# Optimization experiments

Measured on AMD Instinct MI355X. Metric: run time of the kernel, lower is better.

The kernel has to match this reference:

```python
import jax, jax.numpy as jnp
import numpy as np

N_NODES = 50000
N_EDGES = 800000
N_ENT = 500000
N_REL = 500
L = 2          # num_layers
H = 8          # head_num
D = 16         # per-head dim (hidden_dim // head_num)
HID = H * D    # 128
IN = 128       # in_ent_dim == in_rel_dim == hidden_dim
B = 64         # number of graphs in the batch
SLOPE = 0.2    # leaky-relu negative slope


def setup_inputs() -> dict:
    key = jax.random.key(0)
    ks = jax.random.split(key, 11)
    return {
        "ent_table": jax.random.normal(ks[0], (N_ENT, IN), jnp.float32) * 0.05,
        "rel_table": jax.random.normal(ks[1], (N_REL, IN), jnp.float32) * 0.05,
        "W_ent": jax.random.normal(ks[2], (L, IN, HID), jnp.float32) * 0.05,
        "W_rel": jax.random.normal(ks[3], (L, IN, HID), jnp.float32) * 0.05,
        "attn_l": jax.random.normal(ks[4], (L, H, D), jnp.float32) * 0.05,
        "attn_r": jax.random.normal(ks[5], (L, H, D), jnp.float32) * 0.05,
        "attn_e": jax.random.normal(ks[6], (L, H, D), jnp.float32) * 0.05,
        "ent_ids": jax.random.randint(ks[7], (N_NODES,), 0, N_ENT, jnp.int32),
        "rel_ids": jax.random.randint(ks[8], (N_EDGES,), 0, N_REL, jnp.int32),
        "src": jax.random.randint(ks[9], (N_EDGES,), 0, N_NODES, jnp.int32),
        "dst": jax.random.randint(ks[10], (N_EDGES,), 0, N_NODES, jnp.int32),
        # node-0 offset of each subgraph in the batched graph
        "graph_offsets": jnp.arange(B, dtype=jnp.int32) * (N_NODES // B),
    }


def _kge_layer(h, rel_f, src, dst, W_e, W_r, a_l, a_r, a_e):
    # GAT-style relation-aware message passing (KGELayer)
    feat = (h @ W_e).reshape(-1, H, D)        # [N,H,D]
    rfeat = (rel_f @ W_r).reshape(-1, H, D)   # [E,H,D]
    el = jnp.einsum('nhd,hd->nh', feat, a_l)  # src score
    er = jnp.einsum('nhd,hd->nh', feat, a_r)  # dst score
    ee = jnp.einsum('ehd,hd->eh', rfeat, a_e) # relation score
    e = jax.nn.leaky_relu(el[src] + er[dst] + ee, SLOPE)  # [E,H]
    # segment softmax over incoming edges of each dst node
    emax = jax.ops.segment_max(e, dst, num_segments=N_NODES)
    ex = jnp.exp(e - emax[dst])
    denom = jax.ops.segment_sum(ex, dst, num_segments=N_NODES)
    alpha = ex / denom[dst]                   # [E,H]
    msg = (feat[src] + rfeat) * alpha[:, :, None]  # [E,H,D]
    out = jax.ops.segment_sum(msg, dst, num_segments=N_NODES)  # [N,H,D]
    return out.reshape(-1, HID)


def reference(ent_table, rel_table, W_ent, W_rel, attn_l, attn_r, attn_e,
              ent_ids, rel_ids, src, dst, graph_offsets):
    h = ent_table[ent_ids]       # [N,IN]
    rel_f = rel_table[rel_ids]   # [E,IN]
    for l in range(L):
        h = _kge_layer(h, rel_f, src, dst, W_ent[l], W_rel[l],
                       attn_l[l], attn_r[l], attn_e[l])
    # CLS embedding: node 0 of each unbatched subgraph
    return h[graph_offsets]      # [B,HID]
```

## Files before the change

kernel.cpp:

```cpp
#include <hip/hip_runtime.h>
#include <hip/hip_bf16.h>


#define NN   50000
#define NE   800000
#define NR   500
#define HH   8
#define DD   16
#define HIDD 128
#define BB   64

#define MAXS1 16448
#define MAXS0 50000
#define MAXD1 256
#define MAXD2 256


__global__ void k_init(int* slot2, int* slot1, int* slot0, int* c1, int* c2,
                       int* counters) {
    int i = blockIdx.x * blockDim.x + threadIdx.x;
    int stride = gridDim.x * blockDim.x;
    for (int n = i; n < NN; n += stride) { slot2[n] = -1; slot1[n] = -1; slot0[n] = -1; }
    for (int n = i; n < MAXS1; n += stride) c1[n] = 0;
    if (i < BB) c2[i] = 0;
    if (i < 8) counters[i] = 0;
}

__global__ void k_seed(const int* goffs, int* slot2, int* slot1, int* nodesS1,
                       int* counters) {
    int i = threadIdx.x;
    if (i < BB) {
        int n = goffs[i];
        slot2[n] = i;
        slot1[n] = -2;
        nodesS1[i] = n;
    }
    if (i == 0) counters[0] = BB;
}

#define NBUF 512
__global__ void k_scan(const int* __restrict__ src, const int* __restrict__ dst,
                       const int* __restrict__ slotHit, int* __restrict__ slotNew,
                       int* __restrict__ ebuck, int maxd, int* __restrict__ cursor,
                       int* nodes, int nodesCap, int* counters, int cntN) {
    __shared__ int lN[NBUF];
    __shared__ int cNsh, baseN;
    if (threadIdx.x == 0) cNsh = 0;
    __syncthreads();
    int per = (NE + gridDim.x - 1) / gridDim.x;
    int lo = blockIdx.x * per;
    int hi = lo + per; if (hi > NE) hi = NE;
    for (int base = lo; base < hi; base += blockDim.x) {
        int e = base + threadIdx.x;
        if (e < hi) {
            int d = dst[e];
            int slot = slotHit[d];
            if (slot >= 0) {
                int pos = atomicAdd(&cursor[slot], 1);
                if (pos < maxd) ebuck[slot * maxd + pos] = e;
                int s = src[e];
                int old = atomicCAS(&slotNew[s], -1, -2);
                if (old == -1) {
                    int p2 = atomicAdd(&cNsh, 1);
                    lN[p2] = s;
                }
            }
        }
        __syncthreads();
        if (cNsh >= NBUF - 256) {
            int nN = cNsh;
            if (threadIdx.x == 0) baseN = atomicAdd(&counters[cntN], nN);
            __syncthreads();
            for (int i = threadIdx.x; i < nN; i += blockDim.x) {
                int g = baseN + i; if (g < nodesCap) nodes[g] = lN[i];
            }
            __syncthreads();
            if (threadIdx.x == 0) cNsh = 0;
        }
        __syncthreads();
    }
    int nN = cNsh;
    if (threadIdx.x == 0) baseN = atomicAdd(&counters[cntN], nN);
    __syncthreads();
    for (int i = threadIdx.x; i < nN; i += blockDim.x) {
        int g = baseN + i; if (g < nodesCap) nodes[g] = lN[i];
    }
}

__global__ void k_finS1(int* slot1, const int* nodesS1, int* slot0, int* nodesS0,
                        int* counters) {
    int k = blockIdx.x * blockDim.x + threadIdx.x;
    int cnt = counters[0]; if (cnt > MAXS1) cnt = MAXS1;
    if (k < cnt) {
        int n = nodesS1[k];
        slot1[n] = k;
        slot0[n] = -2;
        nodesS0[k] = n;
    }
    if (k == 0) counters[1] = cnt;
}

#define RELB 1000
#define FT 8
__global__ void k_relfeat0(const float* rel_table, const float* __restrict__ W_rel,
                           const float* attn_e, float* rproj, float* ee,
                           const int* nodesS0, const int* counters, const int* ent_ids,
                           const float* __restrict__ ent_table, const float* __restrict__ W_ent,
                           const float* __restrict__ attn_l, const float* __restrict__ attn_r,
                           float* feat0, float* el0, float* er0, int* slot0) {
    int t = threadIdx.x;
    __shared__ float sh[FT][HIDD];
    if (blockIdx.x < RELB) {
        int b = blockIdx.x;
        int l = b / NR, r = b % NR;
        sh[0][t] = rel_table[r * HIDD + t];
        __syncthreads();
        const float* W = W_rel + l * HIDD * HIDD;
        float acc = 0.f;
        for (int j = 0; j < HIDD; j++) acc += sh[0][j] * W[j * HIDD + t];
        rproj[(l * NR + r) * HIDD + t] = acc;
        sh[1][t] = acc;
        __syncthreads();
        if (t < HH) {
            float s = 0.f;
            #pragma unroll
            for (int d = 0; d < DD; d++) s += sh[1][t * DD + d] * attn_e[(l * HH + t) * DD + d];
            ee[(l * NR + r) * HH + t] = s;
        }
        return;
    }
    int cnt = counters[1]; if (cnt > MAXS0) cnt = MAXS0;
    int nTiles = (cnt + FT - 1) / FT;
    int gstride = gridDim.x - RELB;
    for (int tile = blockIdx.x - RELB; tile < nTiles; tile += gstride) {
        int k0 = tile * FT;
        #pragma unroll
        for (int m = 0; m < FT; m++) {
            int k = k0 + m;
            int n = nodesS0[k < cnt ? k : 0];
            if (k < cnt && t == 0) slot0[n] = k;
            sh[m][t] = ent_table[(long)ent_ids[n] * HIDD + t];
        }
        __syncthreads();
        float acc[FT];
        #pragma unroll
        for (int m = 0; m < FT; m++) acc[m] = 0.f;
        for (int j = 0; j < HIDD; j++) {
            float w = W_ent[j * HIDD + t];
            #pragma unroll
            for (int m = 0; m < FT; m++) acc[m] += sh[m][j] * w;
        }
        __syncthreads();
        #pragma unroll
        for (int m = 0; m < FT; m++) {
            int k = k0 + m;
            if (k < cnt) feat0[k * HIDD + t] = acc[m];
            sh[m][t] = acc[m];
        }
        __syncthreads();
        {
            int m = t >> 4, idx = t & 15, h = idx >> 1, isR = idx & 1;
            int k = k0 + m;
            if (k < cnt) {
                const float* av = (isR ? attn_r : attn_l) + h * DD;
                float s = 0.f;
                #pragma unroll
                for (int d = 0; d < DD; d++) s += sh[m][h * DD + d] * av[d];
                if (isR) er0[k * HH + h] = s; else el0[k * HH + h] = s;
            }
        }
        __syncthreads();
    }
}

__global__ void k_layer1(const int* counters,
                         const int* __restrict__ c1, const int* __restrict__ ebuck1,
                         const int* __restrict__ src, const int* __restrict__ rel_ids,
                         const int* __restrict__ slot0,
                         const float* __restrict__ feat0, const float* __restrict__ rproj0,
                         const float* __restrict__ el0, const float* __restrict__ er0,
                         const float* __restrict__ ee0,
                         const float* __restrict__ W_ent1,
                         const float* attn_l1, const float* attn_r1,
                         float* feat1, float* el1, float* er1) {
    int t = threadIdx.x;
    int h = t >> 4;
    int cnt = counters[0]; if (cnt > MAXS1) cnt = MAXS1;
    __shared__ int   eks[MAXD1];
    __shared__ int   erid[MAXD1];
    __shared__ float exsh[MAXD1 * HH];
    __shared__ float row[HIDD];
    __shared__ float f[HIDD];
    for (int k = blockIdx.x; k < cnt; k += gridDim.x) {
        int deg = c1[k]; if (deg > MAXD1) deg = MAXD1;
        for (int i = t; i < deg; i += blockDim.x) {
            int e = ebuck1[k * MAXD1 + i];
            eks[i]  = slot0[src[e]];
            erid[i] = rel_ids[e];
        }
        __syncthreads();
        for (int idx = t; idx < deg * HH; idx += blockDim.x) {
            int i = idx >> 3, hh = idx & 7;
            float sc = el0[eks[i] * HH + hh] + er0[k * HH + hh] + ee0[erid[i] * HH + hh];
            sc = sc >= 0.f ? sc : 0.2f * sc;
            exsh[idx] = expf(sc);
        }
        __syncthreads();
        float acc = 0.f, den = 0.f;
        #pragma unroll 4
        for (int i = 0; i < deg; i++) {
            float ex = exsh[i * HH + h];
            acc += (feat0[eks[i] * HIDD + t] + rproj0[erid[i] * HIDD + t]) * ex;
            den += ex;
        }
        row[t] = den > 0.f ? acc / den : 0.f;
        __syncthreads();
        float a2 = 0.f;
        for (int j = 0; j < HIDD; j++) a2 += row[j] * W_ent1[j * HIDD + t];
        feat1[k * HIDD + t] = a2;
        f[t] = a2;
        __syncthreads();
        if (t < HH) {
            float s = 0.f;
            #pragma unroll
            for (int d = 0; d < DD; d++) s += f[t * DD + d] * attn_l1[t * DD + d];
            el1[k * HH + t] = s;
        } else if (t < 2 * HH) {
            int hh = t - HH;
            float s = 0.f;
            #pragma unroll
            for (int d = 0; d < DD; d++) s += f[hh * DD + d] * attn_r1[hh * DD + d];
            er1[k * HH + hh] = s;
        }
        __syncthreads();
    }
}

__global__ void k_layer2(const int* __restrict__ c2, const int* __restrict__ ebuck2,
                         const int* __restrict__ src, const int* __restrict__ rel_ids,
                         const int* __restrict__ slot1,
                         const float* __restrict__ feat1, const float* __restrict__ rproj1,
                         const float* __restrict__ el1, const float* __restrict__ er1,
                         const float* __restrict__ ee1,
                         float* out) {
    int g = blockIdx.x;
    int t = threadIdx.x;
    int h = t >> 4;
    __shared__ int   eks[MAXD2];
    __shared__ int   erid[MAXD2];
    __shared__ float exsh[MAXD2 * HH];
    int deg = c2[g]; if (deg > MAXD2) deg = MAXD2;
    for (int i = t; i < deg; i += blockDim.x) {
        int e = ebuck2[g * MAXD2 + i];
        eks[i]  = slot1[src[e]];
        erid[i] = rel_ids[e];
    }
    __syncthreads();
    for (int idx = t; idx < deg * HH; idx += blockDim.x) {
        int i = idx >> 3, hh = idx & 7;
        float sc = el1[eks[i] * HH + hh] + er1[g * HH + hh] + ee1[erid[i] * HH + hh];
        sc = sc >= 0.f ? sc : 0.2f * sc;
        exsh[idx] = expf(sc);
    }
    __syncthreads();
    float acc = 0.f, den = 0.f;
    #pragma unroll 4
    for (int i = 0; i < deg; i++) {
        float ex = exsh[i * HH + h];
        acc += (feat1[eks[i] * HIDD + t] + rproj1[erid[i] * HIDD + t]) * ex;
        den += ex;
    }
    out[g * HIDD + t] = den > 0.f ? acc / den : 0.f;
}

extern "C" void kernel_launch(void* const* d_in, const int* in_sizes, int n_in,
                              void* d_out, int out_size, void* d_ws, size_t ws_size,
                              hipStream_t stream) {
    const float* ent_table = (const float*)d_in[0];
    const float* rel_table = (const float*)d_in[1];
    const float* W_ent     = (const float*)d_in[2];
    const float* W_rel     = (const float*)d_in[3];
    const float* attn_l    = (const float*)d_in[4];
    const float* attn_r    = (const float*)d_in[5];
    const float* attn_e    = (const float*)d_in[6];
    const int*   ent_ids   = (const int*)d_in[7];
    const int*   rel_ids   = (const int*)d_in[8];
    const int*   src       = (const int*)d_in[9];
    const int*   dst       = (const int*)d_in[10];
    const int*   goffs     = (const int*)d_in[11];
    float*       out       = (float*)d_out;

    char* p = (char*)d_ws;
    auto alloc = [&](size_t nbytes) {
        void* q = (void*)p;
        p += (nbytes + 255) & ~(size_t)255;
        return q;
    };
    float* rproj   = (float*)alloc((size_t)2 * NR * HIDD * 4);
    float* ee      = (float*)alloc((size_t)2 * NR * HH * 4);
    int*   slot2   = (int*)alloc((size_t)NN * 4);
    int*   slot1   = (int*)alloc((size_t)NN * 4);
    int*   slot0   = (int*)alloc((size_t)NN * 4);
    int*   nodesS1 = (int*)alloc((size_t)MAXS1 * 4);
    int*   nodesS0 = (int*)alloc((size_t)MAXS0 * 4);
    int*   counters= (int*)alloc(8 * 4);
    int*   c1      = (int*)alloc((size_t)MAXS1 * 4);
    int*   c2      = (int*)alloc((size_t)BB * 4);
    int*   ebuck1  = (int*)alloc((size_t)MAXS1 * MAXD1 * 4);
    int*   ebuck2  = (int*)alloc((size_t)BB * MAXD2 * 4);
    float* feat0   = (float*)alloc((size_t)MAXS0 * HIDD * 4);
    float* el0     = (float*)alloc((size_t)MAXS0 * HH * 4);
    float* er0     = (float*)alloc((size_t)MAXS0 * HH * 4);
    float* feat1   = (float*)alloc((size_t)MAXS1 * HIDD * 4);
    float* el1     = (float*)alloc((size_t)MAXS1 * HH * 4);
    float* er1     = (float*)alloc((size_t)MAXS1 * HH * 4);

    const float* rproj0 = rproj;
    const float* rproj1 = rproj + (size_t)NR * HIDD;
    const float* ee0 = ee;
    const float* ee1 = ee + (size_t)NR * HH;
    const float* W_ent0 = W_ent;
    const float* W_ent1 = W_ent + HIDD * HIDD;
    const float* attn_l0 = attn_l, *attn_l1 = attn_l + HH * DD;
    const float* attn_r0 = attn_r, *attn_r1 = attn_r + HH * DD;

    hipLaunchKernelGGL(k_init, dim3(256), dim3(256), 0, stream,
                       slot2, slot1, slot0, c1, c2, counters);
    hipLaunchKernelGGL(k_seed, dim3(1), dim3(64), 0, stream,
                       goffs, slot2, slot1, nodesS1, counters);
    hipLaunchKernelGGL(k_scan, dim3(512), dim3(256), 0, stream,
                       src, dst, slot2, slot1, ebuck2, MAXD2, c2,
                       nodesS1, MAXS1, counters, 0);
    hipLaunchKernelGGL(k_finS1, dim3((MAXS1 + 255) / 256), dim3(256), 0, stream,
                       slot1, nodesS1, slot0, nodesS0, counters);
    hipLaunchKernelGGL(k_scan, dim3(512), dim3(256), 0, stream,
                       src, dst, slot1, slot0, ebuck1, MAXD1, c1,
                       nodesS0, MAXS0, counters, 1);
    hipLaunchKernelGGL(k_relfeat0, dim3(RELB + 1048), dim3(HIDD), 0, stream,
                       rel_table, W_rel, attn_e, rproj, ee,
                       nodesS0, counters, ent_ids, ent_table, W_ent0,
                       attn_l0, attn_r0, feat0, el0, er0, slot0);
    hipLaunchKernelGGL(k_layer1, dim3(1024), dim3(HIDD), 0, stream,
                       counters, c1, ebuck1, src, rel_ids, slot0,
                       feat0, rproj0, el0, er0, ee0, W_ent1, attn_l1, attn_r1,
                       feat1, el1, er1);
    hipLaunchKernelGGL(k_layer2, dim3(BB), dim3(HIDD), 0, stream,
                       c2, ebuck2, src, rel_ids, slot1,
                       feat1, rproj1, el1, er1, ee1, out);
}
```

Measured before the change: 400.9 us.

## Fuse all stages into one persistent cooperative kernel with grid syncs

Replaces eight separate kernel launches with a single cooperative persistent kernel that separates phases with grid-wide syncs. It also finds first-hop destinations by binary search over the graph offsets instead of a slot2 table. Slot assignment now happens inside the scan flush, which removes the finS1 pass and merges the node lists into one array. Each 256-thread block processes two rows per phase. This removes launch overhead and the inter-kernel gaps, but the grid size is capped by occupancy, grid.sync costs time, and shared memory per block grows.

```diff
diff --git a/kernel.cpp b/kernel.cpp
--- a/kernel.cpp
+++ b/kernel.cpp
@@ -1,5 +1,7 @@
 #include <hip/hip_runtime.h>
-#include <hip/hip_bf16.h>
+#include <hip/hip_cooperative_groups.h>
+
+namespace cg = cooperative_groups;
 
 
 #define NN   50000
@@ -14,263 +16,308 @@
 #define MAXS0 50000
 #define MAXD1 256
 #define MAXD2 256
-
-
-__global__ void k_init(int* slot2, int* slot1, int* slot0, int* c1, int* c2,
-                       int* counters) {
-    int i = blockIdx.x * blockDim.x + threadIdx.x;
-    int stride = gridDim.x * blockDim.x;
-    for (int n = i; n < NN; n += stride) { slot2[n] = -1; slot1[n] = -1; slot0[n] = -1; }
-    for (int n = i; n < MAXS1; n += stride) c1[n] = 0;
-    if (i < BB) c2[i] = 0;
-    if (i < 8) counters[i] = 0;
-}
-
-__global__ void k_seed(const int* goffs, int* slot2, int* slot1, int* nodesS1,
-                       int* counters) {
-    int i = threadIdx.x;
-    if (i < BB) {
-        int n = goffs[i];
-        slot2[n] = i;
-        slot1[n] = -2;
-        nodesS1[i] = n;
-    }
-    if (i == 0) counters[0] = BB;
-}
-
-#define NBUF 512
-__global__ void k_scan(const int* __restrict__ src, const int* __restrict__ dst,
-                       const int* __restrict__ slotHit, int* __restrict__ slotNew,
-                       int* __restrict__ ebuck, int maxd, int* __restrict__ cursor,
-                       int* nodes, int nodesCap, int* counters, int cntN) {
-    __shared__ int lN[NBUF];
-    __shared__ int cNsh, baseN;
-    if (threadIdx.x == 0) cNsh = 0;
-    __syncthreads();
-    int per = (NE + gridDim.x - 1) / gridDim.x;
-    int lo = blockIdx.x * per;
-    int hi = lo + per; if (hi > NE) hi = NE;
-    for (int base = lo; base < hi; base += blockDim.x) {
-        int e = base + threadIdx.x;
-        if (e < hi) {
-            int d = dst[e];
-            int slot = slotHit[d];
-            if (slot >= 0) {
-                int pos = atomicAdd(&cursor[slot], 1);
-                if (pos < maxd) ebuck[slot * maxd + pos] = e;
-                int s = src[e];
-                int old = atomicCAS(&slotNew[s], -1, -2);
-                if (old == -1) {
-                    int p2 = atomicAdd(&cNsh, 1);
-                    lN[p2] = s;
-                }
-            }
-        }
-        __syncthreads();
-        if (cNsh >= NBUF - 256) {
-            int nN = cNsh;
-            if (threadIdx.x == 0) baseN = atomicAdd(&counters[cntN], nN);
-            __syncthreads();
-            for (int i = threadIdx.x; i < nN; i += blockDim.x) {
-                int g = baseN + i; if (g < nodesCap) nodes[g] = lN[i];
-            }
-            __syncthreads();
-            if (threadIdx.x == 0) cNsh = 0;
-        }
-        __syncthreads();
-    }
-    int nN = cNsh;
-    if (threadIdx.x == 0) baseN = atomicAdd(&counters[cntN], nN);
-    __syncthreads();
-    for (int i = threadIdx.x; i < nN; i += blockDim.x) {
-        int g = baseN + i; if (g < nodesCap) nodes[g] = lN[i];
-    }
-}
-
-__global__ void k_finS1(int* slot1, const int* nodesS1, int* slot0, int* nodesS0,
-                        int* counters) {
-    int k = blockIdx.x * blockDim.x + threadIdx.x;
-    int cnt = counters[0]; if (cnt > MAXS1) cnt = MAXS1;
-    if (k < cnt) {
-        int n = nodesS1[k];
-        slot1[n] = k;
-        slot0[n] = -2;
-        nodesS0[k] = n;
-    }
-    if (k == 0) counters[1] = cnt;
-}
-
-#define RELB 1000
-#define FT 8
-__global__ void k_relfeat0(const float* rel_table, const float* __restrict__ W_rel,
-                           const float* attn_e, float* rproj, float* ee,
-                           const int* nodesS0, const int* counters, const int* ent_ids,
-                           const float* __restrict__ ent_table, const float* __restrict__ W_ent,
-                           const float* __restrict__ attn_l, const float* __restrict__ attn_r,
-                           float* feat0, float* el0, float* er0, int* slot0) {
-    int t = threadIdx.x;
+#define NBUF  512
+#define FT    8
+#define GRID  1024
+#define TPB   256
+
+#define VREAD(x) (*((volatile int*)&(x)))
+
+
+__global__ __launch_bounds__(TPB, 4)
+void k_fused(const float* __restrict__ ent_table, const float* __restrict__ rel_table,
+             const float* __restrict__ W_ent, const float* __restrict__ W_rel,
+             const float* __restrict__ attn_l, const float* __restrict__ attn_r,
+             const float* __restrict__ attn_e,
+             const int* __restrict__ ent_ids, const int* __restrict__ rel_ids,
+             const int* __restrict__ src, const int* __restrict__ dst,
+             const int* __restrict__ goffs,
+             float* __restrict__ out,
+             float* __restrict__ rproj, float* __restrict__ ee,
+             int* __restrict__ slot1, int* __restrict__ slot0,
+             int* __restrict__ nodes, int* __restrict__ counters,
+             int* __restrict__ c1, int* __restrict__ c2,
+             int* __restrict__ ebuck1, int* __restrict__ ebuck2,
+             float* __restrict__ feat0, float* __restrict__ el0, float* __restrict__ er0,
+             float* __restrict__ feat1, float* __restrict__ el1, float* __restrict__ er1)
+{
+    cg::grid_group grid = cg::this_grid();
+    const int t = threadIdx.x, b = blockIdx.x;
+    const int gsz = gridDim.x;
+    const int gtid = b * TPB + t, gstr = gsz * TPB;
+
+    __shared__ int   lN[NBUF];
+    __shared__ int   cNsh, baseN;
+    __shared__ int   goffsSh[BB];
     __shared__ float sh[FT][HIDD];
-    if (blockIdx.x < RELB) {
-        int b = blockIdx.x;
-        int l = b / NR, r = b % NR;
-        sh[0][t] = rel_table[r * HIDD + t];
-        __syncthreads();
-        const float* W = W_rel + l * HIDD * HIDD;
+    __shared__ int   eks[2][MAXD1];
+    __shared__ int   erid[2][MAXD1];
+    __shared__ float exsh[2][MAXD1 * HH];
+    __shared__ float rowf[2][HIDD];
+    __shared__ float ff[2][HIDD];
+
+    const float* W_ent1  = W_ent  + HIDD * HIDD;
+    const float* attn_l1 = attn_l + HH * DD;
+    const float* attn_r1 = attn_r + HH * DD;
+    const float* rproj0  = rproj;
+    const float* rproj1  = rproj + (size_t)NR * HIDD;
+    const float* ee0     = ee;
+    const float* ee1     = ee + (size_t)NR * HH;
+
+    for (int n = gtid; n < NN; n += gstr) { slot1[n] = -1; slot0[n] = -1; }
+    for (int n = gtid; n < MAXS1; n += gstr) c1[n] = 0;
+    if (gtid < BB) c2[gtid] = 0;
+    if (gtid < 8) counters[gtid] = 0;
+    grid.sync();
+
+    if (b == 0) {
+        if (t < BB) { int n = goffs[t]; slot1[n] = t; slot0[n] = t; nodes[t] = n; }
+        if (t == 0) counters[0] = BB;
+    }
+    if (b < NR) {
+        int half = t >> 7, tc = t & 127;
+        int p = b * 2 + half;
+        int l = p / NR;
+        sh[half][tc] = rel_table[(p % NR) * HIDD + tc];
+        __syncthreads();
+        const float* W = W_rel + (size_t)l * HIDD * HIDD;
         float acc = 0.f;
-        for (int j = 0; j < HIDD; j++) acc += sh[0][j] * W[j * HIDD + t];
-        rproj[(l * NR + r) * HIDD + t] = acc;
-        sh[1][t] = acc;
-        __syncthreads();
-        if (t < HH) {
+        for (int j = 0; j < HIDD; j++) acc += sh[half][j] * W[j * HIDD + tc];
+        rproj[(size_t)p * HIDD + tc] = acc;
+        sh[2 + half][tc] = acc;
+        __syncthreads();
+        if (tc < HH) {
             float s = 0.f;
             #pragma unroll
-            for (int d = 0; d < DD; d++) s += sh[1][t * DD + d] * attn_e[(l * HH + t) * DD + d];
-            ee[(l * NR + r) * HH + t] = s;
-        }
-        return;
-    }
-    int cnt = counters[1]; if (cnt > MAXS0) cnt = MAXS0;
-    int nTiles = (cnt + FT - 1) / FT;
-    int gstride = gridDim.x - RELB;
-    for (int tile = blockIdx.x - RELB; tile < nTiles; tile += gstride) {
-        int k0 = tile * FT;
-        #pragma unroll
-        for (int m = 0; m < FT; m++) {
-            int k = k0 + m;
-            int n = nodesS0[k < cnt ? k : 0];
-            if (k < cnt && t == 0) slot0[n] = k;
-            sh[m][t] = ent_table[(long)ent_ids[n] * HIDD + t];
-        }
-        __syncthreads();
-        float acc[FT];
-        #pragma unroll
-        for (int m = 0; m < FT; m++) acc[m] = 0.f;
-        for (int j = 0; j < HIDD; j++) {
-            float w = W_ent[j * HIDD + t];
+            for (int d = 0; d < DD; d++)
+                s += sh[2 + half][tc * DD + d] * attn_e[(l * HH + tc) * DD + d];
+            ee[p * HH + tc] = s;
+        }
+    }
+    grid.sync();
+
+    if (t < BB) goffsSh[t] = goffs[t];
+    if (t == 0) cNsh = 0;
+    __syncthreads();
+    {
+        int per = (NE + gsz - 1) / gsz;
+        int lo = b * per, hi = lo + per; if (hi > NE) hi = NE;
+        for (int base = lo; base < hi; base += TPB) {
+            int e = base + t;
+            if (e < hi) {
+                int d = dst[e];
+                int loI = 0;
+                if (goffsSh[32] <= d) loI = 32;
+                if (goffsSh[loI + 16] <= d) loI += 16;
+                if (goffsSh[loI + 8]  <= d) loI += 8;
+                if (goffsSh[loI + 4]  <= d) loI += 4;
+                if (goffsSh[loI + 2]  <= d) loI += 2;
+                if (goffsSh[loI + 1]  <= d) loI += 1;
+                if (goffsSh[loI] == d) {
+                    int g = loI;
+                    int pos = atomicAdd(&c2[g], 1);
+                    if (pos < MAXD2) ebuck2[g * MAXD2 + pos] = e;
+                    int s = src[e];
+                    if (atomicCAS(&slot1[s], -1, -2) == -1) {
+                        int p2 = atomicAdd(&cNsh, 1);
+                        lN[p2] = s;
+                    }
+                }
+            }
+            __syncthreads();
+            if (cNsh >= NBUF - TPB) {
+                int nN = cNsh;
+                if (t == 0) baseN = atomicAdd(&counters[0], nN);
+                __syncthreads();
+                for (int i = t; i < nN; i += TPB) {
+                    int pos = baseN + i;
+                    if (pos < MAXS1) { int s = lN[i]; slot1[s] = pos; slot0[s] = pos; nodes[pos] = s; }
+                }
+                __syncthreads();
+                if (t == 0) cNsh = 0;
+            }
+            __syncthreads();
+        }
+        int nN = cNsh;
+        if (t == 0) baseN = atomicAdd(&counters[0], nN);
+        __syncthreads();
+        for (int i = t; i < nN; i += TPB) {
+            int pos = baseN + i;
+            if (pos < MAXS1) { int s = lN[i]; slot1[s] = pos; slot0[s] = pos; nodes[pos] = s; }
+        }
+    }
+    grid.sync();
+
+    int s1cnt = VREAD(counters[0]); if (s1cnt > MAXS1) s1cnt = MAXS1;
+    if (t == 0) cNsh = 0;
+    __syncthreads();
+    {
+        int per = (NE + gsz - 1) / gsz;
+        int lo = b * per, hi = lo + per; if (hi > NE) hi = NE;
+        for (int base = lo; base < hi; base += TPB) {
+            int e = base + t;
+            if (e < hi) {
+                int d = dst[e];
+                int kd = slot1[d];
+                if (kd >= 0) {
+                    int pos = atomicAdd(&c1[kd], 1);
+                    if (pos < MAXD1) ebuck1[kd * MAXD1 + pos] = e;
+                    int s = src[e];
+                    if (atomicCAS(&slot0[s], -1, -2) == -1) {
+                        int p2 = atomicAdd(&cNsh, 1);
+                        lN[p2] = s;
+                    }
+                }
+            }
+            __syncthreads();
+            if (cNsh >= NBUF - TPB) {
+                int nN = cNsh;
+                if (t == 0) baseN = s1cnt + atomicAdd(&counters[1], nN);
+                __syncthreads();
+                for (int i = t; i < nN; i += TPB) {
+                    int pos = baseN + i;
+                    if (pos < MAXS0) { int s = lN[i]; slot0[s] = pos; nodes[pos] = s; }
+                }
+                __syncthreads();
+                if (t == 0) cNsh = 0;
+            }
+            __syncthreads();
+        }
+        int nN = cNsh;
+        if (t == 0) baseN = s1cnt + atomicAdd(&counters[1], nN);
+        __syncthreads();
+        for (int i = t; i < nN; i += TPB) {
+            int pos = baseN + i;
+            if (pos < MAXS0) { int s = lN[i]; slot0[s] = pos; nodes[pos] = s; }
+        }
+    }
+    grid.sync();
+
+    int cnt0 = s1cnt + VREAD(counters[1]); if (cnt0 > MAXS0) cnt0 = MAXS0;
+    {
+        int half = t >> 7, tc = t & 127;
+        int nT = (cnt0 + FT - 1) / FT;
+        for (int tile = b; tile < nT; tile += gsz) {
+            int k0 = tile * FT;
+            for (int m = half; m < FT; m += 2) {
+                int k = k0 + m;
+                int n = nodes[k < cnt0 ? k : 0];
+                sh[m][tc] = ent_table[(long)ent_ids[n] * HIDD + tc];
+            }
+            __syncthreads();
+            float a0 = 0.f, a1 = 0.f, a2 = 0.f, a3 = 0.f;
+            int mb = half * 4;
+            for (int j = 0; j < HIDD; j++) {
+                float w = W_ent[j * HIDD + tc];
+                a0 += sh[mb + 0][j] * w; a1 += sh[mb + 1][j] * w;
+                a2 += sh[mb + 2][j] * w; a3 += sh[mb + 3][j] * w;
+            }
+            __syncthreads();
+            float av4[4] = {a0, a1, a2, a3};
             #pragma unroll
-            for (int m = 0; m < FT; m++) acc[m] += sh[m][j] * w;
-        }
-        __syncthreads();
-        #pragma unroll
-        for (int m = 0; m < FT; m++) {
-            int k = k0 + m;
-            if (k < cnt) feat0[k * HIDD + t] = acc[m];
-            sh[m][t] = acc[m];
-        }
-        __syncthreads();
-        {
-            int m = t >> 4, idx = t & 15, h = idx >> 1, isR = idx & 1;
-            int k = k0 + m;
-            if (k < cnt) {
-                const float* av = (isR ? attn_r : attn_l) + h * DD;
-                float s = 0.f;
-                #pragma unroll
-                for (int d = 0; d < DD; d++) s += sh[m][h * DD + d] * av[d];
-                if (isR) er0[k * HH + h] = s; else el0[k * HH + h] = s;
-            }
-        }
-        __syncthreads();
-    }
-}
-
-__global__ void k_layer1(const int* counters,
-                         const int* __restrict__ c1, const int* __restrict__ ebuck1,
-                         const int* __restrict__ src, const int* __restrict__ rel_ids,
-                         const int* __restrict__ slot0,
-                         const float* __restrict__ feat0, const float* __restrict__ rproj0,
-                         const float* __restrict__ el0, const float* __restrict__ er0,
-                         const float* __restrict__ ee0,
-                         const float* __restrict__ W_ent1,
-                         const float* attn_l1, const float* attn_r1,
-                         float* feat1, float* el1, float* er1) {
-    int t = threadIdx.x;
-    int h = t >> 4;
-    int cnt = counters[0]; if (cnt > MAXS1) cnt = MAXS1;
-    __shared__ int   eks[MAXD1];
-    __shared__ int   erid[MAXD1];
-    __shared__ float exsh[MAXD1 * HH];
-    __shared__ float row[HIDD];
-    __shared__ float f[HIDD];
-    for (int k = blockIdx.x; k < cnt; k += gridDim.x) {
-        int deg = c1[k]; if (deg > MAXD1) deg = MAXD1;
-        for (int i = t; i < deg; i += blockDim.x) {
-            int e = ebuck1[k * MAXD1 + i];
-            eks[i]  = slot0[src[e]];
-            erid[i] = rel_ids[e];
-        }
-        __syncthreads();
-        for (int idx = t; idx < deg * HH; idx += blockDim.x) {
+            for (int mi = 0; mi < 4; mi++) {
+                int k = k0 + mb + mi;
+                if (k < cnt0) feat0[(size_t)k * HIDD + tc] = av4[mi];
+                sh[mb + mi][tc] = av4[mi];
+            }
+            __syncthreads();
+            if (t < 128) {
+                int m = t >> 4, idx = t & 15, hh = idx >> 1, isR = idx & 1;
+                int k = k0 + m;
+                if (k < cnt0) {
+                    const float* av = (isR ? attn_r : attn_l) + hh * DD;
+                    float s = 0.f;
+                    #pragma unroll
+                    for (int d = 0; d < DD; d++) s += sh[m][hh * DD + d] * av[d];
+                    if (isR) er0[k * HH + hh] = s; else el0[k * HH + hh] = s;
+                }
+            }
+            __syncthreads();
+        }
+    }
+    grid.sync();
+
+    {
+        int half = t >> 7, tc = t & 127, h = tc >> 4;
+        for (int kb = b * 2; kb < s1cnt; kb += gsz * 2) {
+            int k = kb + half;
+            bool act = k < s1cnt;
+            int deg = 0;
+            if (act) { deg = c1[k]; if (deg > MAXD1) deg = MAXD1; }
+            for (int i = tc; i < deg; i += 128) {
+                int e = ebuck1[k * MAXD1 + i];
+                eks[half][i]  = slot0[src[e]];
+                erid[half][i] = rel_ids[e];
+            }
+            __syncthreads();
+            for (int idx = tc; idx < deg * HH; idx += 128) {
+                int i = idx >> 3, hh = idx & 7;
+                float sc = el0[eks[half][i] * HH + hh] + er0[k * HH + hh]
+                         + ee0[erid[half][i] * HH + hh];
+                sc = sc >= 0.f ? sc : 0.2f * sc;
+                exsh[half][idx] = expf(sc);
+            }
+            __syncthreads();
+            float acc = 0.f, den = 0.f;
+            for (int i = 0; i < deg; i++) {
+                float ex = exsh[half][i * HH + h];
+                acc += (feat0[(size_t)eks[half][i] * HIDD + tc]
+                      + rproj0[(size_t)erid[half][i] * HIDD + tc]) * ex;
+                den += ex;
+            }
+            rowf[half][tc] = den > 0.f ? acc / den : 0.f;
+            __syncthreads();
+            float a2 = 0.f;
+            for (int j = 0; j < HIDD; j++) a2 += rowf[half][j] * W_ent1[j * HIDD + tc];
+            if (act) feat1[(size_t)k * HIDD + tc] = a2;
+            ff[half][tc] = a2;
+            __syncthreads();
+            if (act) {
+                if (tc < HH) {
+                    float s = 0.f;
+                    #pragma unroll
+                    for (int d = 0; d < DD; d++) s += ff[half][tc * DD + d] * attn_l1[tc * DD + d];
+                    el1[k * HH + tc] = s;
+                } else if (tc < 2 * HH) {
+                    int hh = tc - HH;
+                    float s = 0.f;
+                    #pragma unroll
+                    for (int d = 0; d < DD; d++) s += ff[half][hh * DD + d] * attn_r1[hh * DD + d];
+                    er1[k * HH + hh] = s;
+                }
+            }
+            __syncthreads();
+        }
+    }
+    grid.sync();
+
+    if (b < BB / 2) {
+        int half = t >> 7, tc = t & 127, h = tc >> 4;
+        int g = b * 2 + half;
+        int deg = c2[g]; if (deg > MAXD2) deg = MAXD2;
+        for (int i = tc; i < deg; i += 128) {
+            int e = ebuck2[g * MAXD2 + i];
+            eks[half][i]  = slot1[src[e]];
+            erid[half][i] = rel_ids[e];
+        }
+        __syncthreads();
+        for (int idx = tc; idx < deg * HH; idx += 128) {
             int i = idx >> 3, hh = idx & 7;
-            float sc = el0[eks[i] * HH + hh] + er0[k * HH + hh] + ee0[erid[i] * HH + hh];
+            float sc = el1[eks[half][i] * HH + hh] + er1[g * HH + hh]
+                     + ee1[erid[half][i] * HH + hh];
             sc = sc >= 0.f ? sc : 0.2f * sc;
-            exsh[idx] = expf(sc);
+            exsh[half][idx] = expf(sc);
         }
         __syncthreads();
         float acc = 0.f, den = 0.f;
-        #pragma unroll 4
         for (int i = 0; i < deg; i++) {
-            float ex = exsh[i * HH + h];
-            acc += (feat0[eks[i] * HIDD + t] + rproj0[erid[i] * HIDD + t]) * ex;
+            float ex = exsh[half][i * HH + h];
+            acc += (feat1[(size_t)eks[half][i] * HIDD + tc]
+                  + rproj1[(size_t)erid[half][i] * HIDD + tc]) * ex;
             den += ex;
         }
-        row[t] = den > 0.f ? acc / den : 0.f;
-        __syncthreads();
-        float a2 = 0.f;
-        for (int j = 0; j < HIDD; j++) a2 += row[j] * W_ent1[j * HIDD + t];
-        feat1[k * HIDD + t] = a2;
-        f[t] = a2;
-        __syncthreads();
-        if (t < HH) {
-            float s = 0.f;
-            #pragma unroll
-            for (int d = 0; d < DD; d++) s += f[t * DD + d] * attn_l1[t * DD + d];
-            el1[k * HH + t] = s;
-        } else if (t < 2 * HH) {
-            int hh = t - HH;
-            float s = 0.f;
-            #pragma unroll
-            for (int d = 0; d < DD; d++) s += f[hh * DD + d] * attn_r1[hh * DD + d];
-            er1[k * HH + hh] = s;
-        }
-        __syncthreads();
-    }
-}
-
-__global__ void k_layer2(const int* __restrict__ c2, const int* __restrict__ ebuck2,
-                         const int* __restrict__ src, const int* __restrict__ rel_ids,
-                         const int* __restrict__ slot1,
-                         const float* __restrict__ feat1, const float* __restrict__ rproj1,
-                         const float* __restrict__ el1, const float* __restrict__ er1,
-                         const float* __restrict__ ee1,
-                         float* out) {
-    int g = blockIdx.x;
-    int t = threadIdx.x;
-    int h = t >> 4;
-    __shared__ int   eks[MAXD2];
-    __shared__ int   erid[MAXD2];
-    __shared__ float exsh[MAXD2 * HH];
-    int deg = c2[g]; if (deg > MAXD2) deg = MAXD2;
-    for (int i = t; i < deg; i += blockDim.x) {
-        int e = ebuck2[g * MAXD2 + i];
-        eks[i]  = slot1[src[e]];
-        erid[i] = rel_ids[e];
-    }
-    __syncthreads();
-    for (int idx = t; idx < deg * HH; idx += blockDim.x) {
-        int i = idx >> 3, hh = idx & 7;
-        float sc = el1[eks[i] * HH + hh] + er1[g * HH + hh] + ee1[erid[i] * HH + hh];
-        sc = sc >= 0.f ? sc : 0.2f * sc;
-        exsh[idx] = expf(sc);
-    }
-    __syncthreads();
-    float acc = 0.f, den = 0.f;
-    #pragma unroll 4
-    for (int i = 0; i < deg; i++) {
-        float ex = exsh[i * HH + h];
-        acc += (feat1[eks[i] * HIDD + t] + rproj1[erid[i] * HIDD + t]) * ex;
-        den += ex;
-    }
-    out[g * HIDD + t] = den > 0.f ? acc / den : 0.f;
+        out[g * HIDD + tc] = den > 0.f ? acc / den : 0.f;
+    }
 }
 
 extern "C" void kernel_launch(void* const* d_in, const int* in_sizes, int n_in,
@@ -298,11 +345,9 @@
     };
     float* rproj   = (float*)alloc((size_t)2 * NR * HIDD * 4);
     float* ee      = (float*)alloc((size_t)2 * NR * HH * 4);
-    int*   slot2   = (int*)alloc((size_t)NN * 4);
     int*   slot1   = (int*)alloc((size_t)NN * 4);
     int*   slot0   = (int*)alloc((size_t)NN * 4);
-    int*   nodesS1 = (int*)alloc((size_t)MAXS1 * 4);
-    int*   nodesS0 = (int*)alloc((size_t)MAXS0 * 4);
+    int*   nodes   = (int*)alloc((size_t)MAXS0 * 4);
     int*   counters= (int*)alloc(8 * 4);
     int*   c1      = (int*)alloc((size_t)MAXS1 * 4);
     int*   c2      = (int*)alloc((size_t)BB * 4);
@@ -315,36 +360,30 @@
     float* el1     = (float*)alloc((size_t)MAXS1 * HH * 4);
     float* er1     = (float*)alloc((size_t)MAXS1 * HH * 4);
 
-    const float* rproj0 = rproj;
-    const float* rproj1 = rproj + (size_t)NR * HIDD;
-    const float* ee0 = ee;
-    const float* ee1 = ee + (size_t)NR * HH;
-    const float* W_ent0 = W_ent;
-    const float* W_ent1 = W_ent + HIDD * HIDD;
-    const float* attn_l0 = attn_l, *attn_l1 = attn_l + HH * DD;
-    const float* attn_r0 = attn_r, *attn_r1 = attn_r + HH * DD;
-
-    hipLaunchKernelGGL(k_init, dim3(256), dim3(256), 0, stream,
-                       slot2, slot1, slot0, c1, c2, counters);
-    hipLaunchKernelGGL(k_seed, dim3(1), dim3(64), 0, stream,
-                       goffs, slot2, slot1, nodesS1, counters);
-    hipLaunchKernelGGL(k_scan, dim3(512), dim3(256), 0, stream,
-                       src, dst, slot2, slot1, ebuck2, MAXD2, c2,
-                       nodesS1, MAXS1, counters, 0);
-    hipLaunchKernelGGL(k_finS1, dim3((MAXS1 + 255) / 256), dim3(256), 0, stream,
-                       slot1, nodesS1, slot0, nodesS0, counters);
-    hipLaunchKernelGGL(k_scan, dim3(512), dim3(256), 0, stream,
-                       src, dst, slot1, slot0, ebuck1, MAXD1, c1,
-                       nodesS0, MAXS0, counters, 1);
-    hipLaunchKernelGGL(k_relfeat0, dim3(RELB + 1048), dim3(HIDD), 0, stream,
-                       rel_table, W_rel, attn_e, rproj, ee,
-                       nodesS0, counters, ent_ids, ent_table, W_ent0,
-                       attn_l0, attn_r0, feat0, el0, er0, slot0);
-    hipLaunchKernelGGL(k_layer1, dim3(1024), dim3(HIDD), 0, stream,
-                       counters, c1, ebuck1, src, rel_ids, slot0,
-                       feat0, rproj0, el0, er0, ee0, W_ent1, attn_l1, attn_r1,
-                       feat1, el1, er1);
-    hipLaunchKernelGGL(k_layer2, dim3(BB), dim3(HIDD), 0, stream,
-                       c2, ebuck2, src, rel_ids, slot1,
-                       feat1, rproj1, el1, er1, ee1, out);
+    static int s_grid = 0;
+    if (s_grid == 0) {
+        int nb = 0;
+        if (hipOccupancyMaxActiveBlocksPerMultiprocessor(&nb, k_fused, TPB, 0) != hipSuccess || nb <= 0)
+            nb = 4;
+        hipDeviceProp_t prop;
+        int cu = 256;
+        if (hipGetDeviceProperties(&prop, 0) == hipSuccess) cu = prop.multiProcessorCount;
+        int cap = nb * cu;
+        s_grid = cap < GRID ? cap : GRID;
+        if (s_grid < 64) s_grid = 64;
+    }
+
+    void* args[] = {
+        (void*)&ent_table, (void*)&rel_table, (void*)&W_ent, (void*)&W_rel,
+        (void*)&attn_l, (void*)&attn_r, (void*)&attn_e,
+        (void*)&ent_ids, (void*)&rel_ids, (void*)&src, (void*)&dst, (void*)&goffs,
+        (void*)&out,
+        (void*)&rproj, (void*)&ee,
+        (void*)&slot1, (void*)&slot0, (void*)&nodes, (void*)&counters,
+        (void*)&c1, (void*)&c2, (void*)&ebuck1, (void*)&ebuck2,
+        (void*)&feat0, (void*)&el0, (void*)&er0,
+        (void*)&feat1, (void*)&el1, (void*)&er1
+    };
+    hipLaunchCooperativeKernel((void*)k_fused, dim3(s_grid), dim3(TPB),
+                               args, 0, stream);
 }
```

Result: slower. 884.4 us (+120.6%).

## Merge frontier-building kernels and fold seeding, slot assignment into scans

Applied to the files above, without the earlier changes.

Reduces the launch chain from eight kernels to six. Seeding and the relation projection move into the init kernel, and the first scan finds CLS destinations with a binary search over the graph offsets held in shared memory instead of a slot table. Slot indices are written directly during the scans, which removes the finalize kernel and the slot writes in the feature kernel. A single shared node list is used, with the layer-0 frontier appended after the layer-1 nodes. This trims launch gaps and extra passes, at the cost of more branching in the scans and more complex counter handling.

```diff
diff --git a/kernel.cpp b/kernel.cpp
--- a/kernel.cpp
+++ b/kernel.cpp
@@ -14,131 +14,191 @@
 #define MAXS0 50000
 #define MAXD1 256
 #define MAXD2 256
-
-
-__global__ void k_init(int* slot2, int* slot1, int* slot0, int* c1, int* c2,
-                       int* counters) {
-    int i = blockIdx.x * blockDim.x + threadIdx.x;
-    int stride = gridDim.x * blockDim.x;
-    for (int n = i; n < NN; n += stride) { slot2[n] = -1; slot1[n] = -1; slot0[n] = -1; }
+#define NBUF  512
+#define FT    8
+#define TPB   256
+
+
+__device__ __forceinline__ int cls_lookup(const int* goffsSh, int n) {
+    int lo = 0;
+    if (goffsSh[32] <= n) lo = 32;
+    if (goffsSh[lo + 16] <= n) lo += 16;
+    if (goffsSh[lo + 8]  <= n) lo += 8;
+    if (goffsSh[lo + 4]  <= n) lo += 4;
+    if (goffsSh[lo + 2]  <= n) lo += 2;
+    if (goffsSh[lo + 1]  <= n) lo += 1;
+    return goffsSh[lo] == n ? lo : -1;
+}
+
+#define RELB 500
+__global__ void k_init(const int* __restrict__ goffs,
+                       const float* __restrict__ rel_table,
+                       const float* __restrict__ W_rel,
+                       const float* __restrict__ attn_e,
+                       float* __restrict__ rproj, float* __restrict__ ee,
+                       int* __restrict__ slot1, int* __restrict__ slot0,
+                       int* __restrict__ nodes,
+                       int* __restrict__ c1, int* __restrict__ c2,
+                       int* __restrict__ counters) {
+    int b = blockIdx.x, t = threadIdx.x;
+    if (b < RELB) {
+        __shared__ float sh[4][HIDD];
+        int half = t >> 7, tc = t & 127;
+        int p = b * 2 + half;
+        int l = p / NR;
+        sh[half][tc] = rel_table[(p % NR) * HIDD + tc];
+        __syncthreads();
+        const float* W = W_rel + (size_t)l * HIDD * HIDD;
+        float acc = 0.f;
+        for (int j = 0; j < HIDD; j++) acc += sh[half][j] * W[j * HIDD + tc];
+        rproj[(size_t)p * HIDD + tc] = acc;
+        sh[2 + half][tc] = acc;
+        __syncthreads();
+        if (tc < HH) {
+            float s = 0.f;
+            #pragma unroll
+            for (int d = 0; d < DD; d++)
+                s += sh[2 + half][tc * DD + d] * attn_e[(l * HH + tc) * DD + d];
+            ee[p * HH + tc] = s;
+        }
+        return;
+    }
+    __shared__ int goffsSh[BB];
+    if (t < BB) goffsSh[t] = goffs[t];
+    __syncthreads();
+    int nb = gridDim.x - RELB;
+    int i = (b - RELB) * TPB + t, stride = nb * TPB;
+    for (int n = i; n < NN; n += stride) {
+        int g = cls_lookup(goffsSh, n);
+        slot1[n] = g; slot0[n] = g;
+        if (g >= 0) nodes[g] = n;
+    }
     for (int n = i; n < MAXS1; n += stride) c1[n] = 0;
     if (i < BB) c2[i] = 0;
-    if (i < 8) counters[i] = 0;
-}
-
-__global__ void k_seed(const int* goffs, int* slot2, int* slot1, int* nodesS1,
-                       int* counters) {
-    int i = threadIdx.x;
-    if (i < BB) {
-        int n = goffs[i];
-        slot2[n] = i;
-        slot1[n] = -2;
-        nodesS1[i] = n;
-    }
-    if (i == 0) counters[0] = BB;
-}
-
-#define NBUF 512
-__global__ void k_scan(const int* __restrict__ src, const int* __restrict__ dst,
-                       const int* __restrict__ slotHit, int* __restrict__ slotNew,
-                       int* __restrict__ ebuck, int maxd, int* __restrict__ cursor,
-                       int* nodes, int nodesCap, int* counters, int cntN) {
+    if (i < 8) counters[i] = (i == 0) ? BB : 0;
+}
+
+__global__ void k_scan2(const int* __restrict__ src, const int* __restrict__ dst,
+                        const int* __restrict__ goffs,
+                        int* __restrict__ slot1, int* __restrict__ slot0,
+                        int* __restrict__ nodes,
+                        int* __restrict__ c2, int* __restrict__ ebuck2,
+                        int* __restrict__ counters) {
     __shared__ int lN[NBUF];
     __shared__ int cNsh, baseN;
-    if (threadIdx.x == 0) cNsh = 0;
-    __syncthreads();
-    int per = (NE + gridDim.x - 1) / gridDim.x;
-    int lo = blockIdx.x * per;
-    int hi = lo + per; if (hi > NE) hi = NE;
-    for (int base = lo; base < hi; base += blockDim.x) {
-        int e = base + threadIdx.x;
+    __shared__ int goffsSh[BB];
+    int t = threadIdx.x;
+    if (t < BB) goffsSh[t] = goffs[t];
+    if (t == 0) cNsh = 0;
+    __syncthreads();
+    int gsz = gridDim.x;
+    int per = (NE + gsz - 1) / gsz;
+    int lo = blockIdx.x * per, hi = lo + per; if (hi > NE) hi = NE;
+    for (int base = lo; base < hi; base += TPB) {
+        int e = base + t;
         if (e < hi) {
-            int d = dst[e];
-            int slot = slotHit[d];
-            if (slot >= 0) {
-                int pos = atomicAdd(&cursor[slot], 1);
-                if (pos < maxd) ebuck[slot * maxd + pos] = e;
+            int g = cls_lookup(goffsSh, dst[e]);
+            if (g >= 0) {
+                int pos = atomicAdd(&c2[g], 1);
+                if (pos < MAXD2) ebuck2[g * MAXD2 + pos] = e;
                 int s = src[e];
-                int old = atomicCAS(&slotNew[s], -1, -2);
-                if (old == -1) {
+                if (atomicCAS(&slot1[s], -1, -2) == -1) {
                     int p2 = atomicAdd(&cNsh, 1);
-                    lN[p2] = s;
+                    if (p2 < NBUF) lN[p2] = s;
                 }
             }
         }
         __syncthreads();
-        if (cNsh >= NBUF - 256) {
-            int nN = cNsh;
-            if (threadIdx.x == 0) baseN = atomicAdd(&counters[cntN], nN);
+        if (cNsh >= NBUF - TPB) {
+            int nN = cNsh; if (nN > NBUF) nN = NBUF;
+            if (t == 0) baseN = atomicAdd(&counters[0], nN);
             __syncthreads();
-            for (int i = threadIdx.x; i < nN; i += blockDim.x) {
-                int g = baseN + i; if (g < nodesCap) nodes[g] = lN[i];
+            for (int i = t; i < nN; i += TPB) {
+                int pos = baseN + i;
+                if (pos < MAXS1) { int s = lN[i]; slot1[s] = pos; slot0[s] = pos; nodes[pos] = s; }
             }
             __syncthreads();
-            if (threadIdx.x == 0) cNsh = 0;
-        }
-        __syncthreads();
-    }
-    int nN = cNsh;
-    if (threadIdx.x == 0) baseN = atomicAdd(&counters[cntN], nN);
-    __syncthreads();
-    for (int i = threadIdx.x; i < nN; i += blockDim.x) {
-        int g = baseN + i; if (g < nodesCap) nodes[g] = lN[i];
-    }
-}
-
-__global__ void k_finS1(int* slot1, const int* nodesS1, int* slot0, int* nodesS0,
-                        int* counters) {
-    int k = blockIdx.x * blockDim.x + threadIdx.x;
-    int cnt = counters[0]; if (cnt > MAXS1) cnt = MAXS1;
-    if (k < cnt) {
-        int n = nodesS1[k];
-        slot1[n] = k;
-        slot0[n] = -2;
-        nodesS0[k] = n;
-    }
-    if (k == 0) counters[1] = cnt;
-}
-
-#define RELB 1000
-#define FT 8
-__global__ void k_relfeat0(const float* rel_table, const float* __restrict__ W_rel,
-                           const float* attn_e, float* rproj, float* ee,
-                           const int* nodesS0, const int* counters, const int* ent_ids,
-                           const float* __restrict__ ent_table, const float* __restrict__ W_ent,
-                           const float* __restrict__ attn_l, const float* __restrict__ attn_r,
-                           float* feat0, float* el0, float* er0, int* slot0) {
+            if (t == 0) cNsh = 0;
+        }
+        __syncthreads();
+    }
+    int nN = cNsh; if (nN > NBUF) nN = NBUF;
+    if (t == 0) baseN = atomicAdd(&counters[0], nN);
+    __syncthreads();
+    for (int i = t; i < nN; i += TPB) {
+        int pos = baseN + i;
+        if (pos < MAXS1) { int s = lN[i]; slot1[s] = pos; slot0[s] = pos; nodes[pos] = s; }
+    }
+}
+
+__global__ void k_scan1(const int* __restrict__ src, const int* __restrict__ dst,
+                        const int* __restrict__ slot1, int* __restrict__ slot0,
+                        int* __restrict__ nodes,
+                        int* __restrict__ c1, int* __restrict__ ebuck1,
+                        int* __restrict__ counters) {
+    __shared__ int lN[NBUF];
+    __shared__ int cNsh, baseN;
     int t = threadIdx.x;
+    int s1cnt = counters[0]; if (s1cnt > MAXS1) s1cnt = MAXS1;
+    if (t == 0) cNsh = 0;
+    __syncthreads();
+    int gsz = gridDim.x;
+    int per = (NE + gsz - 1) / gsz;
+    int lo = blockIdx.x * per, hi = lo + per; if (hi > NE) hi = NE;
+    for (int base = lo; base < hi; base += TPB) {
+        int e = base + t;
+        if (e < hi) {
+            int kd = slot1[dst[e]];
+            if (kd >= 0) {
+                int pos = atomicAdd(&c1[kd], 1);
+                if (pos < MAXD1) ebuck1[kd * MAXD1 + pos] = e;
+                int s = src[e];
+                if (atomicCAS(&slot0[s], -1, -2) == -1) {
+                    int p2 = atomicAdd(&cNsh, 1);
+                    if (p2 < NBUF) lN[p2] = s;
+                }
+            }
+        }
+        __syncthreads();
+        if (cNsh >= NBUF - TPB) {
+            int nN = cNsh; if (nN > NBUF) nN = NBUF;
+            if (t == 0) baseN = s1cnt + atomicAdd(&counters[1], nN);
+            __syncthreads();
+            for (int i = t; i < nN; i += TPB) {
+                int pos = baseN + i;
+                if (pos < MAXS0) { int s = lN[i]; slot0[s] = pos; nodes[pos] = s; }
+            }
+            __syncthreads();
+            if (t == 0) cNsh = 0;
+        }
+        __syncthreads();
+    }
+    int nN = cNsh; if (nN > NBUF) nN = NBUF;
+    if (t == 0) baseN = s1cnt + atomicAdd(&counters[1], nN);
+    __syncthreads();
+    for (int i = t; i < nN; i += TPB) {
+        int pos = baseN + i;
+        if (pos < MAXS0) { int s = lN[i]; slot0[s] = pos; nodes[pos] = s; }
+    }
+}
+
+__global__ void k_feat0(const int* __restrict__ nodes, const int* __restrict__ counters,
+                        const int* __restrict__ ent_ids,
+                        const float* __restrict__ ent_table, const float* __restrict__ W_ent,
+                        const float* __restrict__ attn_l, const float* __restrict__ attn_r,
+                        float* __restrict__ feat0, float* __restrict__ el0,
+                        float* __restrict__ er0) {
+    int t = threadIdx.x;
+    int s1 = counters[0]; if (s1 > MAXS1) s1 = MAXS1;
+    int cnt = s1 + counters[1]; if (cnt > MAXS0) cnt = MAXS0;
     __shared__ float sh[FT][HIDD];
-    if (blockIdx.x < RELB) {
-        int b = blockIdx.x;
-        int l = b / NR, r = b % NR;
-        sh[0][t] = rel_table[r * HIDD + t];
-        __syncthreads();
-        const float* W = W_rel + l * HIDD * HIDD;
-        float acc = 0.f;
-        for (int j = 0; j < HIDD; j++) acc += sh[0][j] * W[j * HIDD + t];
-        rproj[(l * NR + r) * HIDD + t] = acc;
-        sh[1][t] = acc;
-        __syncthreads();
-        if (t < HH) {
-            float s = 0.f;
-            #pragma unroll
-            for (int d = 0; d < DD; d++) s += sh[1][t * DD + d] * attn_e[(l * HH + t) * DD + d];
-            ee[(l * NR + r) * HH + t] = s;
-        }
-        return;
-    }
-    int cnt = counters[1]; if (cnt > MAXS0) cnt = MAXS0;
-    int nTiles = (cnt + FT - 1) / FT;
-    int gstride = gridDim.x - RELB;
-    for (int tile = blockIdx.x - RELB; tile < nTiles; tile += gstride) {
+    int nT = (cnt + FT - 1) / FT;
+    for (int tile = blockIdx.x; tile < nT; tile += gridDim.x) {
         int k0 = tile * FT;
         #pragma unroll
         for (int m = 0; m < FT; m++) {
             int k = k0 + m;
-            int n = nodesS0[k < cnt ? k : 0];
-            if (k < cnt && t == 0) slot0[n] = k;
+            int n = nodes[k < cnt ? k : 0];
             sh[m][t] = ent_table[(long)ent_ids[n] * HIDD + t];
         }
         __syncthreads();
@@ -154,7 +214,7 @@
         #pragma unroll
         for (int m = 0; m < FT; m++) {
             int k = k0 + m;
-            if (k < cnt) feat0[k * HIDD + t] = acc[m];
+            if (k < cnt) feat0[(size_t)k * HIDD + t] = acc[m];
             sh[m][t] = acc[m];
         }
         __syncthreads();
@@ -173,7 +233,7 @@
     }
 }
 
-__global__ void k_layer1(const int* counters,
+__global__ void k_layer1(const int* __restrict__ counters,
                          const int* __restrict__ c1, const int* __restrict__ ebuck1,
                          const int* __restrict__ src, const int* __restrict__ rel_ids,
                          const int* __restrict__ slot0,
@@ -181,8 +241,9 @@
                          const float* __restrict__ el0, const float* __restrict__ er0,
                          const float* __restrict__ ee0,
                          const float* __restrict__ W_ent1,
-                         const float* attn_l1, const float* attn_r1,
-                         float* feat1, float* el1, float* er1) {
+                         const float* __restrict__ attn_l1, const float* __restrict__ attn_r1,
+                         float* __restrict__ feat1, float* __restrict__ el1,
+                         float* __restrict__ er1) {
     int t = threadIdx.x;
     int h = t >> 4;
     int cnt = counters[0]; if (cnt > MAXS1) cnt = MAXS1;
@@ -193,13 +254,13 @@
     __shared__ float f[HIDD];
     for (int k = blockIdx.x; k < cnt; k += gridDim.x) {
         int deg = c1[k]; if (deg > MAXD1) deg = MAXD1;
-        for (int i = t; i < deg; i += blockDim.x) {
+        for (int i = t; i < deg; i += 128) {
             int e = ebuck1[k * MAXD1 + i];
             eks[i]  = slot0[src[e]];
             erid[i] = rel_ids[e];
         }
         __syncthreads();
-        for (int idx = t; idx < deg * HH; idx += blockDim.x) {
+        for (int idx = t; idx < deg * HH; idx += 128) {
             int i = idx >> 3, hh = idx & 7;
             float sc = el0[eks[i] * HH + hh] + er0[k * HH + hh] + ee0[erid[i] * HH + hh];
             sc = sc >= 0.f ? sc : 0.2f * sc;
@@ -210,14 +271,15 @@
         #pragma unroll 4
         for (int i = 0; i < deg; i++) {
             float ex = exsh[i * HH + h];
-            acc += (feat0[eks[i] * HIDD + t] + rproj0[erid[i] * HIDD + t]) * ex;
+            acc += (feat0[(size_t)eks[i] * HIDD + t]
+                  + rproj0[(size_t)erid[i] * HIDD + t]) * ex;
             den += ex;
         }
         row[t] = den > 0.f ? acc / den : 0.f;
         __syncthreads();
         float a2 = 0.f;
         for (int j = 0; j < HIDD; j++) a2 += row[j] * W_ent1[j * HIDD + t];
-        feat1[k * HIDD + t] = a2;
+        feat1[(size_t)k * HIDD + t] = a2;
         f[t] = a2;
         __syncthreads();
         if (t < HH) {
@@ -242,7 +304,7 @@
                          const float* __restrict__ feat1, const float* __restrict__ rproj1,
                          const float* __restrict__ el1, const float* __restrict__ er1,
                          const float* __restrict__ ee1,
-                         float* out) {
+                         float* __restrict__ out) {
     int g = blockIdx.x;
     int t = threadIdx.x;
     int h = t >> 4;
@@ -250,13 +312,13 @@
     __shared__ int   erid[MAXD2];
     __shared__ float exsh[MAXD2 * HH];
     int deg = c2[g]; if (deg > MAXD2) deg = MAXD2;
-    for (int i = t; i < deg; i += blockDim.x) {
+    for (int i = t; i < deg; i += 128) {
         int e = ebuck2[g * MAXD2 + i];
         eks[i]  = slot1[src[e]];
         erid[i] = rel_ids[e];
     }
     __syncthreads();
-    for (int idx = t; idx < deg * HH; idx += blockDim.x) {
+    for (int idx = t; idx < deg * HH; idx += 128) {
         int i = idx >> 3, hh = idx & 7;
         float sc = el1[eks[i] * HH + hh] + er1[g * HH + hh] + ee1[erid[i] * HH + hh];
         sc = sc >= 0.f ? sc : 0.2f * sc;
@@ -267,7 +329,8 @@
     #pragma unroll 4
     for (int i = 0; i < deg; i++) {
         float ex = exsh[i * HH + h];
-        acc += (feat1[eks[i] * HIDD + t] + rproj1[erid[i] * HIDD + t]) * ex;
+        acc += (feat1[(size_t)eks[i] * HIDD + t]
+              + rproj1[(size_t)erid[i] * HIDD + t]) * ex;
         den += ex;
     }
     out[g * HIDD + t] = den > 0.f ? acc / den : 0.f;
@@ -298,11 +361,9 @@
     };
     float* rproj   = (float*)alloc((size_t)2 * NR * HIDD * 4);
     float* ee      = (float*)alloc((size_t)2 * NR * HH * 4);
-    int*   slot2   = (int*)alloc((size_t)NN * 4);
     int*   slot1   = (int*)alloc((size_t)NN * 4);
     int*   slot0   = (int*)alloc((size_t)NN * 4);
-    int*   nodesS1 = (int*)alloc((size_t)MAXS1 * 4);
-    int*   nodesS0 = (int*)alloc((size_t)MAXS0 * 4);
+    int*   nodes   = (int*)alloc((size_t)MAXS0 * 4);
     int*   counters= (int*)alloc(8 * 4);
     int*   c1      = (int*)alloc((size_t)MAXS1 * 4);
     int*   c2      = (int*)alloc((size_t)BB * 4);
@@ -321,25 +382,19 @@
     const float* ee1 = ee + (size_t)NR * HH;
     const float* W_ent0 = W_ent;
     const float* W_ent1 = W_ent + HIDD * HIDD;
-    const float* attn_l0 = attn_l, *attn_l1 = attn_l + HH * DD;
-    const float* attn_r0 = attn_r, *attn_r1 = attn_r + HH * DD;
-
-    hipLaunchKernelGGL(k_init, dim3(256), dim3(256), 0, stream,
-                       slot2, slot1, slot0, c1, c2, counters);
-    hipLaunchKernelGGL(k_seed, dim3(1), dim3(64), 0, stream,
-                       goffs, slot2, slot1, nodesS1, counters);
-    hipLaunchKernelGGL(k_scan, dim3(512), dim3(256), 0, stream,
-                       src, dst, slot2, slot1, ebuck2, MAXD2, c2,
-                       nodesS1, MAXS1, counters, 0);
-    hipLaunchKernelGGL(k_finS1, dim3((MAXS1 + 255) / 256), dim3(256), 0, stream,
-                       slot1, nodesS1, slot0, nodesS0, counters);
-    hipLaunchKernelGGL(k_scan, dim3(512), dim3(256), 0, stream,
-                       src, dst, slot1, slot0, ebuck1, MAXD1, c1,
-                       nodesS0, MAXS0, counters, 1);
-    hipLaunchKernelGGL(k_relfeat0, dim3(RELB + 1048), dim3(HIDD), 0, stream,
-                       rel_table, W_rel, attn_e, rproj, ee,
-                       nodesS0, counters, ent_ids, ent_table, W_ent0,
-                       attn_l0, attn_r0, feat0, el0, er0, slot0);
+    const float* attn_l1 = attn_l + HH * DD;
+    const float* attn_r1 = attn_r + HH * DD;
+
+    hipLaunchKernelGGL(k_init, dim3(RELB + 524), dim3(TPB), 0, stream,
+                       goffs, rel_table, W_rel, attn_e, rproj, ee,
+                       slot1, slot0, nodes, c1, c2, counters);
+    hipLaunchKernelGGL(k_scan2, dim3(1024), dim3(TPB), 0, stream,
+                       src, dst, goffs, slot1, slot0, nodes, c2, ebuck2, counters);
+    hipLaunchKernelGGL(k_scan1, dim3(1024), dim3(TPB), 0, stream,
+                       src, dst, slot1, slot0, nodes, c1, ebuck1, counters);
+    hipLaunchKernelGGL(k_feat0, dim3(1024), dim3(HIDD), 0, stream,
+                       nodes, counters, ent_ids, ent_table, W_ent0,
+                       attn_l, attn_r, feat0, el0, er0);
     hipLaunchKernelGGL(k_layer1, dim3(1024), dim3(HIDD), 0, stream,
                        counters, c1, ebuck1, src, rel_ids, slot0,
                        feat0, rproj0, el0, er0, ee0, W_ent1, attn_l1, attn_r1,
```

New measurement: 399.4 us. No clear change (-0.4%).
